# Kernel optimization log

Hardware: AMD Instinct MI355X
Metric: run time of the kernel (lower is better)

## Reference

```python
import jax, jax.numpy as jnp
import numpy as np

N, D, H, O = 512, 128, 256, 256

def setup_inputs() -> dict:
    key = jax.random.key(0)
    ks = jax.random.split(key, 10)
    s = lambda fan_in: 1.0 / np.sqrt(fan_in)
    return {
        "x": jax.random.normal(ks[0], (N, D), dtype=jnp.float32),
        "adj": jax.random.uniform(ks[1], (N, N), dtype=jnp.float32),
        # mpnn_compute: MLP(2D -> H -> H)
        "W1": jax.random.normal(ks[2], (H, 2 * D), dtype=jnp.float32) * s(2 * D),
        "b1": jnp.zeros((H,), dtype=jnp.float32),
        "W2": jax.random.normal(ks[3], (H, H), dtype=jnp.float32) * s(H),
        "b2": jnp.zeros((H,), dtype=jnp.float32),
        # out_compute: MLP(H -> H -> O)
        "Wo1": jax.random.normal(ks[4], (H, H), dtype=jnp.float32) * s(H),
        "bo1": jnp.zeros((H,), dtype=jnp.float32),
        "Wo2": jax.random.normal(ks[5], (O, H), dtype=jnp.float32) * s(H),
        "bo2": jnp.zeros((O,), dtype=jnp.float32),
    }


def reference(x, adj, W1, b1, W2, b2, Wo1, bo1, Wo2, bo2):
    n, d = x.shape
    # e[i, j] = concat(x[j], x[i]); split W1 so we never materialize the cat:
    # linear_1(e)[i,j] = x[j] @ Wa^T + x[i] @ Wb^T + b1
    Wa = W1[:, :d]   # acts on x[j] (first half of cat = x1 = x broadcast over i)
    Wb = W1[:, d:]   # acts on x[i] (second half = x2)
    pa = x @ Wa.T    # [N, H], indexed by j
    pb = x @ Wb.T    # [N, H], indexed by i
    h = jax.nn.relu(pa[None, :, :] + pb[:, None, :] + b1)  # [N, N, H]
    e = jnp.einsum('ijh,kh->ijk', h, W2) + b2               # [N, N, H]
    pred = jnp.mean(adj[:, :, None] * e, axis=1)            # [N, H]
    # out_compute MLP (normalize_input=False)
    h2 = jax.nn.relu(pred @ Wo1.T + bo1)
    return h2 @ Wo2.T + bo2                                  # [N, O]
```

## Files before the change

kernel.cpp:

```cpp
#include <hip/hip_runtime.h>

#define NN 512
#define DD 128
#define HH 256

__global__ __launch_bounds__(256) void k0_tr(const float* __restrict__ W1,
                                             const float* __restrict__ W2,
                                             const float* __restrict__ Wo1,
                                             const float* __restrict__ Wo2,
                                             float* __restrict__ wsT) {
    __shared__ float tl[64][68];
    const int b = blockIdx.x;
    const int t = threadIdx.x;
    const int m = b >> 4, tile = b & 15;
    const float* src = (m == 0) ? W1 : (m == 1) ? W2 : (m == 2) ? Wo1 : Wo2;
    float* dst = wsT + m * (HH * HH);
    const int sr0 = (tile >> 2) * 64;
    const int sc0 = (tile & 3) * 64;
    const int rr = t >> 4;
    const int cc = (t & 15) * 4;
    #pragma unroll
    for (int it = 0; it < 4; ++it) {
        const int row = rr + 16 * it;
        float4 v = *(const float4*)&src[(sr0 + row) * HH + sc0 + cc];
        tl[row][cc + 0] = v.x;
        tl[row][cc + 1] = v.y;
        tl[row][cc + 2] = v.z;
        tl[row][cc + 3] = v.w;
    }
    __syncthreads();
    #pragma unroll
    for (int it = 0; it < 4; ++it) {
        const int lc = rr + 16 * it;
        float4 o;
        o.x = tl[cc + 0][lc];
        o.y = tl[cc + 1][lc];
        o.z = tl[cc + 2][lc];
        o.w = tl[cc + 3][lc];
        *(float4*)&dst[(sc0 + lc) * HH + sr0 + cc] = o;
    }
}

__global__ __launch_bounds__(256) void k1_papb(const float* __restrict__ x,
                                               const float* __restrict__ W1T,
                                               const float* __restrict__ b1,
                                               float* __restrict__ pa,
                                               float* __restrict__ pbb) {
    __shared__ float xs[2][DD];
    const int b = blockIdx.x;
    const int t = threadIdx.x;
    const int i0 = b * 2;
    if (t < 64) {
        const int f = t * 4;
        *(float4*)&xs[f >> 7][f & 127] = *(const float4*)&x[i0 * DD + f];
    }
    __syncthreads();
    const float* wt = W1T + t;
    const int crot = (b * 8) & 127;
    float pe0 = 0.f, po0 = 0.f, pe1 = 0.f, po1 = 0.f;
    float qe0 = 0.f, qo0 = 0.f, qe1 = 0.f, qo1 = 0.f;
    #pragma unroll 2
    for (int cc0 = 0; cc0 < 128; cc0 += 8) {
        const int c = (cc0 + crot) & 127;
        float w0 = wt[(c + 0) * HH], w1 = wt[(c + 1) * HH];
        float w2 = wt[(c + 2) * HH], w3 = wt[(c + 3) * HH];
        float w4 = wt[(c + 4) * HH], w5 = wt[(c + 5) * HH];
        float w6 = wt[(c + 6) * HH], w7 = wt[(c + 7) * HH];
        float v0 = wt[(128 + c + 0) * HH], v1 = wt[(128 + c + 1) * HH];
        float v2 = wt[(128 + c + 2) * HH], v3 = wt[(128 + c + 3) * HH];
        float v4 = wt[(128 + c + 4) * HH], v5 = wt[(128 + c + 5) * HH];
        float v6 = wt[(128 + c + 6) * HH], v7 = wt[(128 + c + 7) * HH];
        float4 x0a = *(const float4*)&xs[0][c];
        float4 x0b = *(const float4*)&xs[0][c + 4];
        float4 x1a = *(const float4*)&xs[1][c];
        float4 x1b = *(const float4*)&xs[1][c + 4];
        pe0 += w0 * x0a.x + w1 * x0a.y + w2 * x0a.z + w3 * x0a.w;
        po0 += w4 * x0b.x + w5 * x0b.y + w6 * x0b.z + w7 * x0b.w;
        pe1 += w0 * x1a.x + w1 * x1a.y + w2 * x1a.z + w3 * x1a.w;
        po1 += w4 * x1b.x + w5 * x1b.y + w6 * x1b.z + w7 * x1b.w;
        qe0 += v0 * x0a.x + v1 * x0a.y + v2 * x0a.z + v3 * x0a.w;
        qo0 += v4 * x0b.x + v5 * x0b.y + v6 * x0b.z + v7 * x0b.w;
        qe1 += v0 * x1a.x + v1 * x1a.y + v2 * x1a.z + v3 * x1a.w;
        qo1 += v4 * x1b.x + v5 * x1b.y + v6 * x1b.z + v7 * x1b.w;
    }
    const float bb = b1[t];
    pa[i0 * HH + t] = pe0 + po0;
    pa[(i0 + 1) * HH + t] = pe1 + po1;
    pbb[i0 * HH + t] = qe0 + qo0 + bb;
    pbb[(i0 + 1) * HH + t] = qe1 + qo1 + bb;
}

__device__ __forceinline__ void stage_dot8(const float* __restrict__ wt,
                                           const float* in0, const float* in1,
                                           int hrot, float& A0, float& A1) {
    float e0 = 0.f, o0 = 0.f, e1 = 0.f, o1 = 0.f;
    #pragma unroll 2
    for (int hh0 = 0; hh0 < 64; hh0 += 8) {
        const int hh = (hh0 + hrot) & 63;
        float w0 = wt[(hh + 0) * HH], w1 = wt[(hh + 1) * HH];
        float w2 = wt[(hh + 2) * HH], w3 = wt[(hh + 3) * HH];
        float w4 = wt[(hh + 4) * HH], w5 = wt[(hh + 5) * HH];
        float w6 = wt[(hh + 6) * HH], w7 = wt[(hh + 7) * HH];
        float4 t0a = *(const float4*)&in0[hh];
        float4 t0b = *(const float4*)&in0[hh + 4];
        float4 t1a = *(const float4*)&in1[hh];
        float4 t1b = *(const float4*)&in1[hh + 4];
        e0 += w0 * t0a.x + w1 * t0a.y + w2 * t0a.z + w3 * t0a.w;
        o0 += w4 * t0b.x + w5 * t0b.y + w6 * t0b.z + w7 * t0b.w;
        e1 += w0 * t1a.x + w1 * t1a.y + w2 * t1a.z + w3 * t1a.w;
        o1 += w4 * t1b.x + w5 * t1b.y + w6 * t1b.z + w7 * t1b.w;
    }
    A0 = e0 + o0;
    A1 = e1 + o1;
}

__global__ __launch_bounds__(1024) void k2_rest(const float* __restrict__ adj,
                                                const float* __restrict__ pa,
                                                const float* __restrict__ pbb,
                                                const float* __restrict__ wsT,
                                                const float* __restrict__ b2,
                                                const float* __restrict__ bo1,
                                                const float* __restrict__ bo2,
                                                float* __restrict__ out) {
    __shared__ float adjs[2][NN];
    __shared__ float pbbs[2][HH];
    __shared__ float ts[2][HH];
    __shared__ float buf1[2][HH];
    __shared__ float buf2[2][HH];
    __shared__ float redbuf[4096];
    __shared__ float rsum_s[2];

    const int b = blockIdx.x;
    const int t = threadIdx.x;
    const int i0 = b * 2;

    if (t < 256) {
        const int f = t * 4;
        *(float4*)&adjs[f >> 9][f & 511] = *(const float4*)&adj[(i0 + (f >> 9)) * NN + (f & 511)];
    } else if (t < 384) {
        const int f = (t - 256) * 4;
        *(float4*)&pbbs[f >> 8][f & 255] = *(const float4*)&pbb[(i0 + (f >> 8)) * HH + (f & 255)];
    }
    __syncthreads();

    if (t < 128) {
        const int r = t >> 6, l = t & 63;
        float s = 0.f;
        #pragma unroll
        for (int m = 0; m < 8; ++m) s += adjs[r][l + 64 * m];
        #pragma unroll
        for (int off = 32; off > 0; off >>= 1) s += __shfl_down(s, off, 64);
        if (l == 0) rsum_s[r] = s;
    }

    {
        const int hb = t >> 9;
        const int jq = (t >> 7) & 3;
        const int hl = t & 127;
        const int h = hb * 128 + hl;
        const float pb0 = pbbs[0][h];
        const float pb1 = pbbs[1][h];
        const float* pac = pa + (jq * 128) * HH + h;
        const float* arow0 = &adjs[0][jq * 128];
        const float* arow1 = &adjs[1][jq * 128];
        const int jrot = (b * 8) & 127;
        float ae0 = 0.f, ao0 = 0.f, ae1 = 0.f, ao1 = 0.f;
        #pragma unroll 2
        for (int jj0 = 0; jj0 < 128; jj0 += 8) {
            const int j = (jj0 + jrot) & 127;
            float p0 = pac[(j + 0) * HH], p1 = pac[(j + 1) * HH];
            float p2 = pac[(j + 2) * HH], p3 = pac[(j + 3) * HH];
            float p4 = pac[(j + 4) * HH], p5 = pac[(j + 5) * HH];
            float p6 = pac[(j + 6) * HH], p7 = pac[(j + 7) * HH];
            float4 A0a = *(const float4*)&arow0[j];
            float4 A0b = *(const float4*)&arow0[j + 4];
            float4 A1a = *(const float4*)&arow1[j];
            float4 A1b = *(const float4*)&arow1[j + 4];
            float r0 = fmaxf(p0 + pb0, 0.f), r1 = fmaxf(p1 + pb0, 0.f);
            float r2 = fmaxf(p2 + pb0, 0.f), r3 = fmaxf(p3 + pb0, 0.f);
            float r4 = fmaxf(p4 + pb0, 0.f), r5 = fmaxf(p5 + pb0, 0.f);
            float r6 = fmaxf(p6 + pb0, 0.f), r7 = fmaxf(p7 + pb0, 0.f);
            ae0 += A0a.x * r0 + A0a.y * r1 + A0a.z * r2 + A0a.w * r3;
            ao0 += A0b.x * r4 + A0b.y * r5 + A0b.z * r6 + A0b.w * r7;
            float s0 = fmaxf(p0 + pb1, 0.f), s1 = fmaxf(p1 + pb1, 0.f);
            float s2 = fmaxf(p2 + pb1, 0.f), s3 = fmaxf(p3 + pb1, 0.f);
            float s4 = fmaxf(p4 + pb1, 0.f), s5 = fmaxf(p5 + pb1, 0.f);
            float s6 = fmaxf(p6 + pb1, 0.f), s7 = fmaxf(p7 + pb1, 0.f);
            ae1 += A1a.x * s0 + A1a.y * s1 + A1a.z * s2 + A1a.w * s3;
            ao1 += A1b.x * s4 + A1b.y * s5 + A1b.z * s6 + A1b.w * s7;
        }
        const float ac0 = ae0 + ao0;
        const float ac1 = ae1 + ao1;
        redbuf[((jq * 2 + hb) * 2 + 0) * 128 + hl] = ac0;
        redbuf[((jq * 2 + hb) * 2 + 1) * 128 + hl] = ac1;
        __syncthreads();
        if (jq == 0) {
            #pragma unroll
            for (int r = 0; r < 2; ++r) {
                float s = (r == 0 ? ac0 : ac1);
                #pragma unroll
                for (int q = 1; q < 4; ++q)
                    s += redbuf[((q * 2 + hb) * 2 + r) * 128 + hl];
                ts[r][h] = s;
            }
        }
    }
    __syncthreads();

    const int k = t & 255;
    const int hp = t >> 8;
    const int hrot = (b * 8) & 63;
    const float* W2T  = wsT + 1 * (HH * HH);
    const float* Wo1T = wsT + 2 * (HH * HH);
    const float* Wo2T = wsT + 3 * (HH * HH);

    {
        float a0, a1;
        stage_dot8(W2T + (hp * 64) * HH + k, &ts[0][hp * 64], &ts[1][hp * 64], hrot, a0, a1);
        redbuf[(hp * 2 + 0) * 256 + k] = a0;
        redbuf[(hp * 2 + 1) * 256 + k] = a1;
        __syncthreads();
        if (hp == 0) {
            const float bv = b2[k];
            const float inv = 1.0f / (float)NN;
            float s0 = a0, s1 = a1;
            #pragma unroll
            for (int p = 1; p < 4; ++p) {
                s0 += redbuf[(p * 2 + 0) * 256 + k];
                s1 += redbuf[(p * 2 + 1) * 256 + k];
            }
            buf1[0][k] = (s0 + bv * rsum_s[0]) * inv;
            buf1[1][k] = (s1 + bv * rsum_s[1]) * inv;
        }
    }
    __syncthreads();

    {
        float a0, a1;
        stage_dot8(Wo1T + (hp * 64) * HH + k, &buf1[0][hp * 64], &buf1[1][hp * 64], hrot, a0, a1);
        redbuf[(hp * 2 + 0) * 256 + k] = a0;
        redbuf[(hp * 2 + 1) * 256 + k] = a1;
        __syncthreads();
        if (hp == 0) {
            const float bv = bo1[k];
            float s0 = a0, s1 = a1;
            #pragma unroll
            for (int p = 1; p < 4; ++p) {
                s0 += redbuf[(p * 2 + 0) * 256 + k];
                s1 += redbuf[(p * 2 + 1) * 256 + k];
            }
            buf2[0][k] = fmaxf(s0 + bv, 0.f);
            buf2[1][k] = fmaxf(s1 + bv, 0.f);
        }
    }
    __syncthreads();

    {
        float a0, a1;
        stage_dot8(Wo2T + (hp * 64) * HH + k, &buf2[0][hp * 64], &buf2[1][hp * 64], hrot, a0, a1);
        redbuf[(hp * 2 + 0) * 256 + k] = a0;
        redbuf[(hp * 2 + 1) * 256 + k] = a1;
        __syncthreads();
        if (hp == 0) {
            const float bv = bo2[k];
            float s0 = a0, s1 = a1;
            #pragma unroll
            for (int p = 1; p < 4; ++p) {
                s0 += redbuf[(p * 2 + 0) * 256 + k];
                s1 += redbuf[(p * 2 + 1) * 256 + k];
            }
            out[i0 * HH + k] = s0 + bv;
            out[(i0 + 1) * HH + k] = s1 + bv;
        }
    }
}

extern "C" void kernel_launch(void* const* d_in, const int* in_sizes, int n_in,
                              void* d_out, int out_size, void* d_ws, size_t ws_size,
                              hipStream_t stream) {
    const float* x   = (const float*)d_in[0];
    const float* adj = (const float*)d_in[1];
    const float* W1  = (const float*)d_in[2];
    const float* b1  = (const float*)d_in[3];
    const float* W2  = (const float*)d_in[4];
    const float* b2  = (const float*)d_in[5];
    const float* Wo1 = (const float*)d_in[6];
    const float* bo1 = (const float*)d_in[7];
    const float* Wo2 = (const float*)d_in[8];
    const float* bo2 = (const float*)d_in[9];
    float* out = (float*)d_out;
    float* ws  = (float*)d_ws;

    float* wsT = ws;
    float* pa  = ws + 262144;
    float* pbb = ws + 393216;

    k0_tr<<<64, 256, 0, stream>>>(W1, W2, Wo1, Wo2, wsT);
    k1_papb<<<256, 256, 0, stream>>>(x, wsT, b1, pa, pbb);
    k2_rest<<<256, 1024, 0, stream>>>(adj, pa, pbb, wsT, b2, bo1, bo2, out);
}
```

Measured before the change: 32.62 us.

## Process four rows per block in k2_rest to halve pa and weight reloads

Each block of the main kernel now handles four output rows instead of two, and the grid shrinks from 256 to 128 blocks. Every pa element and every weight value loaded from global memory is reused across four rows, which halves total global traffic for the aggregation and MLP stages. The cost is fewer blocks than the device has compute units, which leaves some of the GPU idle, plus more registers per thread and longer per-block latency.

```diff
diff --git a/kernel.cpp b/kernel.cpp
--- a/kernel.cpp
+++ b/kernel.cpp
@@ -90,10 +90,12 @@
     pbb[(i0 + 1) * HH + t] = qe1 + qo1 + bb;
 }
 
-__device__ __forceinline__ void stage_dot8(const float* __restrict__ wt,
-                                           const float* in0, const float* in1,
-                                           int hrot, float& A0, float& A1) {
-    float e0 = 0.f, o0 = 0.f, e1 = 0.f, o1 = 0.f;
+__device__ __forceinline__ void sdot4(const float* __restrict__ wt,
+                                      const float* in0, const float* in1,
+                                      const float* in2, const float* in3,
+                                      int hrot, float& A0, float& A1,
+                                      float& A2, float& A3) {
+    float a0 = 0.f, a1 = 0.f, a2 = 0.f, a3 = 0.f;
     #pragma unroll 2
     for (int hh0 = 0; hh0 < 64; hh0 += 8) {
         const int hh = (hh0 + hrot) & 63;
@@ -101,17 +103,25 @@
         float w2 = wt[(hh + 2) * HH], w3 = wt[(hh + 3) * HH];
         float w4 = wt[(hh + 4) * HH], w5 = wt[(hh + 5) * HH];
         float w6 = wt[(hh + 6) * HH], w7 = wt[(hh + 7) * HH];
-        float4 t0a = *(const float4*)&in0[hh];
-        float4 t0b = *(const float4*)&in0[hh + 4];
-        float4 t1a = *(const float4*)&in1[hh];
-        float4 t1b = *(const float4*)&in1[hh + 4];
-        e0 += w0 * t0a.x + w1 * t0a.y + w2 * t0a.z + w3 * t0a.w;
-        o0 += w4 * t0b.x + w5 * t0b.y + w6 * t0b.z + w7 * t0b.w;
-        e1 += w0 * t1a.x + w1 * t1a.y + w2 * t1a.z + w3 * t1a.w;
-        o1 += w4 * t1b.x + w5 * t1b.y + w6 * t1b.z + w7 * t1b.w;
-    }
-    A0 = e0 + o0;
-    A1 = e1 + o1;
+        float4 tA, tB;
+        tA = *(const float4*)&in0[hh];
+        tB = *(const float4*)&in0[hh + 4];
+        a0 += w0 * tA.x + w1 * tA.y + w2 * tA.z + w3 * tA.w
+            + w4 * tB.x + w5 * tB.y + w6 * tB.z + w7 * tB.w;
+        tA = *(const float4*)&in1[hh];
+        tB = *(const float4*)&in1[hh + 4];
+        a1 += w0 * tA.x + w1 * tA.y + w2 * tA.z + w3 * tA.w
+            + w4 * tB.x + w5 * tB.y + w6 * tB.z + w7 * tB.w;
+        tA = *(const float4*)&in2[hh];
+        tB = *(const float4*)&in2[hh + 4];
+        a2 += w0 * tA.x + w1 * tA.y + w2 * tA.z + w3 * tA.w
+            + w4 * tB.x + w5 * tB.y + w6 * tB.z + w7 * tB.w;
+        tA = *(const float4*)&in3[hh];
+        tB = *(const float4*)&in3[hh + 4];
+        a3 += w0 * tA.x + w1 * tA.y + w2 * tA.z + w3 * tA.w
+            + w4 * tB.x + w5 * tB.y + w6 * tB.z + w7 * tB.w;
+    }
+    A0 = a0; A1 = a1; A2 = a2; A3 = a3;
 }
 
 __global__ __launch_bounds__(1024) void k2_rest(const float* __restrict__ adj,
@@ -122,28 +132,28 @@
                                                 const float* __restrict__ bo1,
                                                 const float* __restrict__ bo2,
                                                 float* __restrict__ out) {
-    __shared__ float adjs[2][NN];
-    __shared__ float pbbs[2][HH];
-    __shared__ float ts[2][HH];
-    __shared__ float buf1[2][HH];
-    __shared__ float buf2[2][HH];
+    __shared__ float adjs[4][NN];
+    __shared__ float pbbs[4][HH];
+    __shared__ float ts[4][HH];
+    __shared__ float buf1[4][HH];
+    __shared__ float buf2[4][HH];
     __shared__ float redbuf[4096];
-    __shared__ float rsum_s[2];
+    __shared__ float rsum_s[4];
 
     const int b = blockIdx.x;
     const int t = threadIdx.x;
-    const int i0 = b * 2;
-
-    if (t < 256) {
+    const int i0 = b * 4;
+
+    if (t < 512) {
         const int f = t * 4;
         *(float4*)&adjs[f >> 9][f & 511] = *(const float4*)&adj[(i0 + (f >> 9)) * NN + (f & 511)];
-    } else if (t < 384) {
-        const int f = (t - 256) * 4;
+    } else if (t < 768) {
+        const int f = (t - 512) * 4;
         *(float4*)&pbbs[f >> 8][f & 255] = *(const float4*)&pbb[(i0 + (f >> 8)) * HH + (f & 255)];
     }
     __syncthreads();
 
-    if (t < 128) {
+    if (t < 256) {
         const int r = t >> 6, l = t & 63;
         float s = 0.f;
         #pragma unroll
@@ -158,13 +168,13 @@
         const int jq = (t >> 7) & 3;
         const int hl = t & 127;
         const int h = hb * 128 + hl;
-        const float pb0 = pbbs[0][h];
-        const float pb1 = pbbs[1][h];
+        const float pbv0 = pbbs[0][h];
+        const float pbv1 = pbbs[1][h];
+        const float pbv2 = pbbs[2][h];
+        const float pbv3 = pbbs[3][h];
         const float* pac = pa + (jq * 128) * HH + h;
-        const float* arow0 = &adjs[0][jq * 128];
-        const float* arow1 = &adjs[1][jq * 128];
         const int jrot = (b * 8) & 127;
-        float ae0 = 0.f, ao0 = 0.f, ae1 = 0.f, ao1 = 0.f;
+        float ac0 = 0.f, ac1 = 0.f, ac2 = 0.f, ac3 = 0.f;
         #pragma unroll 2
         for (int jj0 = 0; jj0 < 128; jj0 += 8) {
             const int j = (jj0 + jrot) & 127;
@@ -172,37 +182,70 @@
             float p2 = pac[(j + 2) * HH], p3 = pac[(j + 3) * HH];
             float p4 = pac[(j + 4) * HH], p5 = pac[(j + 5) * HH];
             float p6 = pac[(j + 6) * HH], p7 = pac[(j + 7) * HH];
-            float4 A0a = *(const float4*)&arow0[j];
-            float4 A0b = *(const float4*)&arow0[j + 4];
-            float4 A1a = *(const float4*)&arow1[j];
-            float4 A1b = *(const float4*)&arow1[j + 4];
-            float r0 = fmaxf(p0 + pb0, 0.f), r1 = fmaxf(p1 + pb0, 0.f);
-            float r2 = fmaxf(p2 + pb0, 0.f), r3 = fmaxf(p3 + pb0, 0.f);
-            float r4 = fmaxf(p4 + pb0, 0.f), r5 = fmaxf(p5 + pb0, 0.f);
-            float r6 = fmaxf(p6 + pb0, 0.f), r7 = fmaxf(p7 + pb0, 0.f);
-            ae0 += A0a.x * r0 + A0a.y * r1 + A0a.z * r2 + A0a.w * r3;
-            ao0 += A0b.x * r4 + A0b.y * r5 + A0b.z * r6 + A0b.w * r7;
-            float s0 = fmaxf(p0 + pb1, 0.f), s1 = fmaxf(p1 + pb1, 0.f);
-            float s2 = fmaxf(p2 + pb1, 0.f), s3 = fmaxf(p3 + pb1, 0.f);
-            float s4 = fmaxf(p4 + pb1, 0.f), s5 = fmaxf(p5 + pb1, 0.f);
-            float s6 = fmaxf(p6 + pb1, 0.f), s7 = fmaxf(p7 + pb1, 0.f);
-            ae1 += A1a.x * s0 + A1a.y * s1 + A1a.z * s2 + A1a.w * s3;
-            ao1 += A1b.x * s4 + A1b.y * s5 + A1b.z * s6 + A1b.w * s7;
-        }
-        const float ac0 = ae0 + ao0;
-        const float ac1 = ae1 + ao1;
-        redbuf[((jq * 2 + hb) * 2 + 0) * 128 + hl] = ac0;
-        redbuf[((jq * 2 + hb) * 2 + 1) * 128 + hl] = ac1;
+            float4 Aa, Ab;
+            {
+                Aa = *(const float4*)&adjs[0][jq * 128 + j];
+                Ab = *(const float4*)&adjs[0][jq * 128 + j + 4];
+                float q0 = fmaxf(p0 + pbv0, 0.f), q1 = fmaxf(p1 + pbv0, 0.f);
+                float q2 = fmaxf(p2 + pbv0, 0.f), q3 = fmaxf(p3 + pbv0, 0.f);
+                float q4 = fmaxf(p4 + pbv0, 0.f), q5 = fmaxf(p5 + pbv0, 0.f);
+                float q6 = fmaxf(p6 + pbv0, 0.f), q7 = fmaxf(p7 + pbv0, 0.f);
+                ac0 += Aa.x * q0 + Aa.y * q1 + Aa.z * q2 + Aa.w * q3
+                     + Ab.x * q4 + Ab.y * q5 + Ab.z * q6 + Ab.w * q7;
+            }
+            {
+                Aa = *(const float4*)&adjs[1][jq * 128 + j];
+                Ab = *(const float4*)&adjs[1][jq * 128 + j + 4];
+                float q0 = fmaxf(p0 + pbv1, 0.f), q1 = fmaxf(p1 + pbv1, 0.f);
+                float q2 = fmaxf(p2 + pbv1, 0.f), q3 = fmaxf(p3 + pbv1, 0.f);
+                float q4 = fmaxf(p4 + pbv1, 0.f), q5 = fmaxf(p5 + pbv1, 0.f);
+                float q6 = fmaxf(p6 + pbv1, 0.f), q7 = fmaxf(p7 + pbv1, 0.f);
+                ac1 += Aa.x * q0 + Aa.y * q1 + Aa.z * q2 + Aa.w * q3
+                     + Ab.x * q4 + Ab.y * q5 + Ab.z * q6 + Ab.w * q7;
+            }
+            {
+                Aa = *(const float4*)&adjs[2][jq * 128 + j];
+                Ab = *(const float4*)&adjs[2][jq * 128 + j + 4];
+                float q0 = fmaxf(p0 + pbv2, 0.f), q1 = fmaxf(p1 + pbv2, 0.f);
+                float q2 = fmaxf(p2 + pbv2, 0.f), q3 = fmaxf(p3 + pbv2, 0.f);
+                float q4 = fmaxf(p4 + pbv2, 0.f), q5 = fmaxf(p5 + pbv2, 0.f);
+                float q6 = fmaxf(p6 + pbv2, 0.f), q7 = fmaxf(p7 + pbv2, 0.f);
+                ac2 += Aa.x * q0 + Aa.y * q1 + Aa.z * q2 + Aa.w * q3
+                     + Ab.x * q4 + Ab.y * q5 + Ab.z * q6 + Ab.w * q7;
+            }
+            {
+                Aa = *(const float4*)&adjs[3][jq * 128 + j];
+                Ab = *(const float4*)&adjs[3][jq * 128 + j + 4];
+                float q0 = fmaxf(p0 + pbv3, 0.f), q1 = fmaxf(p1 + pbv3, 0.f);
+                float q2 = fmaxf(p2 + pbv3, 0.f), q3 = fmaxf(p3 + pbv3, 0.f);
+                float q4 = fmaxf(p4 + pbv3, 0.f), q5 = fmaxf(p5 + pbv3, 0.f);
+                float q6 = fmaxf(p6 + pbv3, 0.f), q7 = fmaxf(p7 + pbv3, 0.f);
+                ac3 += Aa.x * q0 + Aa.y * q1 + Aa.z * q2 + Aa.w * q3
+                     + Ab.x * q4 + Ab.y * q5 + Ab.z * q6 + Ab.w * q7;
+            }
+        }
+        if (jq) {
+            const int base = ((jq - 1) * 2 + hb) * 512;
+            redbuf[base + 0 * 128 + hl] = ac0;
+            redbuf[base + 1 * 128 + hl] = ac1;
+            redbuf[base + 2 * 128 + hl] = ac2;
+            redbuf[base + 3 * 128 + hl] = ac3;
+        }
         __syncthreads();
         if (jq == 0) {
+            float s0 = ac0, s1 = ac1, s2 = ac2, s3 = ac3;
             #pragma unroll
-            for (int r = 0; r < 2; ++r) {
-                float s = (r == 0 ? ac0 : ac1);
-                #pragma unroll
-                for (int q = 1; q < 4; ++q)
-                    s += redbuf[((q * 2 + hb) * 2 + r) * 128 + hl];
-                ts[r][h] = s;
-            }
+            for (int q = 1; q < 4; ++q) {
+                const int base = ((q - 1) * 2 + hb) * 512;
+                s0 += redbuf[base + 0 * 128 + hl];
+                s1 += redbuf[base + 1 * 128 + hl];
+                s2 += redbuf[base + 2 * 128 + hl];
+                s3 += redbuf[base + 3 * 128 + hl];
+            }
+            ts[0][h] = s0;
+            ts[1][h] = s1;
+            ts[2][h] = s2;
+            ts[3][h] = s3;
         }
     }
     __syncthreads();
@@ -215,62 +258,89 @@
     const float* Wo2T = wsT + 3 * (HH * HH);
 
     {
-        float a0, a1;
-        stage_dot8(W2T + (hp * 64) * HH + k, &ts[0][hp * 64], &ts[1][hp * 64], hrot, a0, a1);
-        redbuf[(hp * 2 + 0) * 256 + k] = a0;
-        redbuf[(hp * 2 + 1) * 256 + k] = a1;
+        float a0, a1, a2, a3;
+        sdot4(W2T + (hp * 64) * HH + k, &ts[0][hp * 64], &ts[1][hp * 64],
+              &ts[2][hp * 64], &ts[3][hp * 64], hrot, a0, a1, a2, a3);
+        const int base = (hp * 4) * 256 + k;
+        redbuf[base + 0 * 256] = a0;
+        redbuf[base + 1 * 256] = a1;
+        redbuf[base + 2 * 256] = a2;
+        redbuf[base + 3 * 256] = a3;
         __syncthreads();
         if (hp == 0) {
             const float bv = b2[k];
             const float inv = 1.0f / (float)NN;
-            float s0 = a0, s1 = a1;
+            float s0 = a0, s1 = a1, s2 = a2, s3 = a3;
             #pragma unroll
             for (int p = 1; p < 4; ++p) {
-                s0 += redbuf[(p * 2 + 0) * 256 + k];
-                s1 += redbuf[(p * 2 + 1) * 256 + k];
+                const int pb = (p * 4) * 256 + k;
+                s0 += redbuf[pb + 0 * 256];
+                s1 += redbuf[pb + 1 * 256];
+                s2 += redbuf[pb + 2 * 256];
+                s3 += redbuf[pb + 3 * 256];
             }
             buf1[0][k] = (s0 + bv * rsum_s[0]) * inv;
             buf1[1][k] = (s1 + bv * rsum_s[1]) * inv;
+            buf1[2][k] = (s2 + bv * rsum_s[2]) * inv;
+            buf1[3][k] = (s3 + bv * rsum_s[3]) * inv;
         }
     }
     __syncthreads();
 
     {
-        float a0, a1;
-        stage_dot8(Wo1T + (hp * 64) * HH + k, &buf1[0][hp * 64], &buf1[1][hp * 64], hrot, a0, a1);
-        redbuf[(hp * 2 + 0) * 256 + k] = a0;
-        redbuf[(hp * 2 + 1) * 256 + k] = a1;
+        float a0, a1, a2, a3;
+        sdot4(Wo1T + (hp * 64) * HH + k, &buf1[0][hp * 64], &buf1[1][hp * 64],
+              &buf1[2][hp * 64], &buf1[3][hp * 64], hrot, a0, a1, a2, a3);
+        const int base = (hp * 4) * 256 + k;
+        redbuf[base + 0 * 256] = a0;
+        redbuf[base + 1 * 256] = a1;
+        redbuf[base + 2 * 256] = a2;
+        redbuf[base + 3 * 256] = a3;
         __syncthreads();
         if (hp == 0) {
             const float bv = bo1[k];
-            float s0 = a0, s1 = a1;
+            float s0 = a0, s1 = a1, s2 = a2, s3 = a3;
             #pragma unroll
             for (int p = 1; p < 4; ++p) {
-                s0 += redbuf[(p * 2 + 0) * 256 + k];
-                s1 += redbuf[(p * 2 + 1) * 256 + k];
+                const int pb = (p * 4) * 256 + k;
+                s0 += redbuf[pb + 0 * 256];
+                s1 += redbuf[pb + 1 * 256];
+                s2 += redbuf[pb + 2 * 256];
+                s3 += redbuf[pb + 3 * 256];
             }
             buf2[0][k] = fmaxf(s0 + bv, 0.f);
             buf2[1][k] = fmaxf(s1 + bv, 0.f);
+            buf2[2][k] = fmaxf(s2 + bv, 0.f);
+            buf2[3][k] = fmaxf(s3 + bv, 0.f);
         }
     }
     __syncthreads();
 
     {
-        float a0, a1;
-        stage_dot8(Wo2T + (hp * 64) * HH + k, &buf2[0][hp * 64], &buf2[1][hp * 64], hrot, a0, a1);
-        redbuf[(hp * 2 + 0) * 256 + k] = a0;
-        redbuf[(hp * 2 + 1) * 256 + k] = a1;
+        float a0, a1, a2, a3;
+        sdot4(Wo2T + (hp * 64) * HH + k, &buf2[0][hp * 64], &buf2[1][hp * 64],
+              &buf2[2][hp * 64], &buf2[3][hp * 64], hrot, a0, a1, a2, a3);
+        const int base = (hp * 4) * 256 + k;
+        redbuf[base + 0 * 256] = a0;
+        redbuf[base + 1 * 256] = a1;
+        redbuf[base + 2 * 256] = a2;
+        redbuf[base + 3 * 256] = a3;
         __syncthreads();
         if (hp == 0) {
             const float bv = bo2[k];
-            float s0 = a0, s1 = a1;
+            float s0 = a0, s1 = a1, s2 = a2, s3 = a3;
             #pragma unroll
             for (int p = 1; p < 4; ++p) {
-                s0 += redbuf[(p * 2 + 0) * 256 + k];
-                s1 += redbuf[(p * 2 + 1) * 256 + k];
-            }
-            out[i0 * HH + k] = s0 + bv;
+                const int pb = (p * 4) * 256 + k;
+                s0 += redbuf[pb + 0 * 256];
+                s1 += redbuf[pb + 1 * 256];
+                s2 += redbuf[pb + 2 * 256];
+                s3 += redbuf[pb + 3 * 256];
+            }
+            out[(i0 + 0) * HH + k] = s0 + bv;
             out[(i0 + 1) * HH + k] = s1 + bv;
+            out[(i0 + 2) * HH + k] = s2 + bv;
+            out[(i0 + 3) * HH + k] = s3 + bv;
         }
     }
 }
@@ -297,5 +367,5 @@
 
     k0_tr<<<64, 256, 0, stream>>>(W1, W2, Wo1, Wo2, wsT);
     k1_papb<<<256, 256, 0, stream>>>(x, wsT, b1, pa, pbb);
-    k2_rest<<<256, 1024, 0, stream>>>(adj, pa, pbb, wsT, b2, bo1, bo2, out);
-}
+    k2_rest<<<128, 1024, 0, stream>>>(adj, pa, pbb, wsT, b2, bo1, bo2, out);
+}
```

Measured after the change: 40.86 us. 1.25x slower.
